# Kernel tuning notes

Measured on AMD Instinct MI355X. Metric: run time of the kernel, lower is better.

Reference implementation:

```python
import jax, jax.numpy as jnp
import numpy as np

E = 768   # embedding_dim
D = 64    # head_dim
B = 8
S = 2048


def setup_inputs() -> dict:
    key = jax.random.key(0)
    k1, k2, k3, k4 = jax.random.split(key, 4)
    inputs = jax.random.normal(k1, (B, S, E), dtype=jnp.float32)
    # causal mask: 1 where attending allowed, 0 elsewhere (masked_fill where ==0)
    attention_mask = jnp.tril(jnp.ones((S, S), dtype=jnp.int32))[None, :, :]
    Q = jax.random.normal(k2, (E, D), dtype=jnp.float32) * 0.01
    K = jax.random.normal(k3, (E, D), dtype=jnp.float32) * 0.01
    V = jax.random.normal(k4, (E, D), dtype=jnp.float32) * 0.01
    return {"inputs": inputs, "attention_mask": attention_mask, "Q": Q, "K": K, "V": V}


def reference(inputs, attention_mask, Q, K, V):
    scale = 1.0 / np.sqrt(D).astype(np.float32)
    q = inputs @ Q          # [B,S,D]
    k = inputs @ K          # [B,S,D]
    v = inputs @ V          # [B,S,D]
    w = jnp.einsum('bqd,bkd->bqk', q, k) * scale   # [B,S,S]
    w = jnp.where(attention_mask == 0, -jnp.inf, w)
    attn = jax.nn.softmax(w, axis=-1)              # [B,S,S]
    states = attn @ v                              # [B,S,D] (dropout p=0.0 is identity)
    return states
```

## Files before the change

kernel.cpp:

```cpp
#include <hip/hip_runtime.h>
#include <cstdint>

#define B_ 8
#define S_ 2048
#define E_ 768
#define D_ 64
#define NSPLIT 4
#define SEGLEN (S_ / NSPLIT)
#define ROWS (B_ * S_)

typedef unsigned short ushort_t;
typedef __attribute__((ext_vector_type(8))) short s16x8;
typedef __attribute__((ext_vector_type(4))) float f32x4;

__device__ inline ushort_t f2bf(float f) {
  unsigned int x = __float_as_uint(f);
  return (ushort_t)((x + 0x7fffu + ((x >> 16) & 1u)) >> 16);
}

__device__ inline unsigned int pkbf(float hi, float lo) {
  return __builtin_amdgcn_perm(__float_as_uint(hi) + 0x8000u,
                               __float_as_uint(lo) + 0x8000u, 0x07060302u);
}

__device__ inline void async16(const void* g, void* l) {
  __builtin_amdgcn_global_load_lds(
      (const __attribute__((address_space(1))) unsigned int*)g,
      (__attribute__((address_space(3))) unsigned int*)l, 16, 0, 0);
}

__global__ __launch_bounds__(256) void wt_kernel(
    const float* __restrict__ Wq, const float* __restrict__ Wk,
    const float* __restrict__ Wv, ushort_t* __restrict__ wt) {
  const int mat = blockIdx.y;
  const int e = blockIdx.x * 4 + (threadIdx.x >> 6);
  const int d = threadIdx.x & 63;
  const float* W = (mat == 0) ? Wq : ((mat == 1) ? Wk : Wv);
  wt[(long)(mat * 64 + d) * E_ + e] = f2bf(W[(long)e * D_ + d]);
}

__global__ __launch_bounds__(256) void qkv_mfma(
    const float* __restrict__ in, const ushort_t* __restrict__ wt,
    ushort_t* __restrict__ qb, ushort_t* __restrict__ kb,
    ushort_t* __restrict__ vtb) {
  const int tid = threadIdx.x;
  const int w = tid >> 6;
  const int L = tid & 63;
  const int c = L & 15;
  const int q = L >> 4;
  const int row0 = blockIdx.x * 32;

  __shared__ float Alds[2][32][64];
  __shared__ ushort_t Blds[2][192][64];

  const int ar0 = w * 8 + (L >> 4);
  const int ar1 = ar0 + 4;
  const int asl = L & 15;
  const float* asrc0 = in + (long)(row0 + ar0) * E_ + ((asl ^ (ar0 & 15)) << 2);
  const float* asrc1 = in + (long)(row0 + ar1) * E_ + ((asl ^ (ar1 & 15)) << 2);
  const int bsl = L & 7;
  const ushort_t* bsrc[6];
#pragma unroll
  for (int jj = 0; jj < 6; ++jj) {
    const int br = w * 48 + jj * 8 + (L >> 3);
    bsrc[jj] = wt + (long)br * E_ + ((bsl ^ (br & 7)) << 3);
  }
  float* ad[2] = {&Alds[0][w * 8][0], &Alds[1][w * 8][0]};
  ushort_t* bd[2] = {&Blds[0][w * 48][0], &Blds[1][w * 48][0]};

  const int mloc = w & 1;
  const int nbase = (w >> 1) * 6;
  const int ra = mloc * 16 + c;
  const int offA00 = ra * 256 + ((2 * q + 0) ^ c) * 16;
  const int offA01 = ra * 256 + ((2 * q + 1) ^ c) * 16;
  const int offA10 = ra * 256 + ((8 + 2 * q + 0) ^ c) * 16;
  const int offA11 = ra * 256 + ((8 + 2 * q + 1) ^ c) * 16;
  int offB0[6], offB1[6];
#pragma unroll
  for (int t = 0; t < 6; ++t) {
    const int n = (nbase + t) * 16 + c;
    offB0[t] = n * 128 + ((q + 0) ^ (c & 7)) * 16;
    offB1[t] = n * 128 + ((q + 4) ^ (c & 7)) * 16;
  }
  const char* Abase = (const char*)&Alds[0][0][0];
  const char* Bbase = (const char*)&Blds[0][0][0];

  f32x4 acc[6];
#pragma unroll
  for (int n = 0; n < 6; ++n) acc[n] = (f32x4){0.f, 0.f, 0.f, 0.f};

  async16(asrc0, ad[0]);
  async16(asrc1, ad[0] + 4 * 64);
#pragma unroll
  for (int jj = 0; jj < 6; ++jj) async16(bsrc[jj], bd[0] + jj * 8 * 64);
  asrc0 += 64; asrc1 += 64;
#pragma unroll
  for (int jj = 0; jj < 6; ++jj) bsrc[jj] += 64;

  for (int it = 0; it < E_ / 64; ++it) {
    const int b = it & 1;
    __syncthreads();
    if (it + 1 < E_ / 64) {
      const int nb = 1 - b;
      async16(asrc0, ad[nb]);
      async16(asrc1, ad[nb] + 4 * 64);
#pragma unroll
      for (int jj = 0; jj < 6; ++jj) async16(bsrc[jj], bd[nb] + jj * 8 * 64);
      asrc0 += 64; asrc1 += 64;
#pragma unroll
      for (int jj = 0; jj < 6; ++jj) bsrc[jj] += 64;
    }
    const char* Ab = Abase + b * 8192;
    const char* Bb = Bbase + b * 24576;
    const float4 a00 = *(const float4*)(Ab + offA00);
    const float4 a01 = *(const float4*)(Ab + offA01);
    const float4 a10 = *(const float4*)(Ab + offA10);
    const float4 a11 = *(const float4*)(Ab + offA11);
    union { s16x8 v; unsigned int u[4]; } af0, af1;
    af0.u[0] = pkbf(a00.y, a00.x);
    af0.u[1] = pkbf(a00.w, a00.z);
    af0.u[2] = pkbf(a01.y, a01.x);
    af0.u[3] = pkbf(a01.w, a01.z);
    af1.u[0] = pkbf(a10.y, a10.x);
    af1.u[1] = pkbf(a10.w, a10.z);
    af1.u[2] = pkbf(a11.y, a11.x);
    af1.u[3] = pkbf(a11.w, a11.z);
#pragma unroll
    for (int t = 0; t < 6; ++t) {
      const s16x8 bf0 = *(const s16x8*)(Bb + offB0[t]);
      const s16x8 bf1 = *(const s16x8*)(Bb + offB1[t]);
      acc[t] = __builtin_amdgcn_mfma_f32_16x16x32_bf16(af0.v, bf0, acc[t], 0, 0, 0);
      acc[t] = __builtin_amdgcn_mfma_f32_16x16x32_bf16(af1.v, bf1, acc[t], 0, 0, 0);
    }
  }

  const float qscale = 0.125f * 1.44269504088896340736f;
  const int row0w = row0 + mloc * 16;
  const int b_ = row0w >> 11;
  const int srow = row0w & (S_ - 1);
#pragma unroll
  for (int n = 0; n < 6; ++n) {
    const int gn = nbase + n;
    const int mat = gn >> 2;
    const int d0 = (gn & 3) * 16 + c;
#pragma unroll
    for (int reg = 0; reg < 4; ++reg) {
      const int m = q * 4 + reg;
      const float x = acc[n][reg];
      if (mat == 0) {
        qb[(long)(row0w + m) * D_ + d0] = f2bf(x * qscale);
      } else if (mat == 1) {
        kb[(long)(row0w + m) * D_ + d0] = f2bf(x);
      } else {
        vtb[(long)b_ * D_ * S_ + (long)d0 * S_ + srow + m] = f2bf(x);
      }
    }
  }
}

__global__ __launch_bounds__(256) void attn_mfma(
    const ushort_t* __restrict__ qb, const ushort_t* __restrict__ kb,
    const ushort_t* __restrict__ vtb, float* __restrict__ op,
    float* __restrict__ lw) {
  const int qb0 = blockIdx.x * 64;
  const int batch = blockIdx.y;
  const int seg = blockIdx.z;
  const int j0 = seg * SEGLEN;
  const int jmax = min(j0 + SEGLEN, qb0 + 64);
  if (j0 >= jmax) return;
  const int nt64 = (jmax - j0) >> 6;
  const int niter = (nt64 + 1) >> 1;

  const int w = threadIdx.x >> 6;
  const int L = threadIdx.x & 63;
  const int col = L & 15;
  const int quad = L >> 4;

  __shared__ ushort_t Kl[2][2][64][64];
  __shared__ ushort_t Vl[2][2][64][64];
  __shared__ ushort_t Pl[4][16][72];

  const ushort_t* kbb = kb + (long)batch * S_ * D_;
  const ushort_t* vbb = vtb + (long)batch * D_ * S_;

  const int lr = L >> 3;
  const int gsw = (L & 7) ^ lr;
  const ushort_t* ksrc[4];
  const ushort_t* vsrc[4];
  ushort_t* kdst[2][4];
  ushort_t* vdst[2][4];
#pragma unroll
  for (int jj = 0; jj < 4; ++jj) {
    const int i = w * 4 + jj;
    ksrc[jj] = kbb + (long)(j0 + i * 8 + lr) * D_ + gsw * 8;
    vsrc[jj] = vbb + (long)((i & 7) * 8 + lr) * S_ + j0 + (i >> 3) * 64 + gsw * 8;
    kdst[0][jj] = &Kl[0][0][0][0] + i * 512;
    kdst[1][jj] = &Kl[1][0][0][0] + i * 512;
    vdst[0][jj] = &Vl[0][0][0][0] + i * 512;
    vdst[1][jj] = &Vl[1][0][0][0] + i * 512;
  }

  const int s0 = ((quad ^ (col & 7)) * 16);

  const ushort_t* qrow = qb + ((long)(batch * S_ + qb0 + w * 16 + col) * D_);
  const s16x8 qf0 = *(const s16x8*)(qrow + quad * 8);
  const s16x8 qf1 = *(const s16x8*)(qrow + 32 + quad * 8);

  f32x4 O[4];
#pragma unroll
  for (int t = 0; t < 4; ++t) O[t] = (f32x4){0.f, 0.f, 0.f, 0.f};
  float l[4] = {0.f, 0.f, 0.f, 0.f};

#pragma unroll
  for (int jj = 0; jj < 4; ++jj) {
    async16(ksrc[jj], kdst[0][jj]);
    async16(vsrc[jj], vdst[0][jj]);
    ksrc[jj] += 128 * D_;
    vsrc[jj] += 128;
  }

  for (int it = 0; it < niter; ++it) {
    const int b = it & 1;
    __syncthreads();
    if (it + 1 < niter) {
      const int nb = 1 - b;
#pragma unroll
      for (int jj = 0; jj < 4; ++jj) {
        async16(ksrc[jj], kdst[nb][jj]);
        async16(vsrc[jj], vdst[nb][jj]);
        ksrc[jj] += 128 * D_;
        vsrc[jj] += 128;
      }
    }
#pragma unroll
    for (int h = 0; h < 2; ++h) {
      const int t64 = it * 2 + h;
      if (t64 < nt64) {
        const int kt = j0 + t64 * 64;
        const char* Kb = (const char*)&Kl[b][h][0][0];
        const char* Vb = (const char*)&Vl[b][h][0][0];
        f32x4 S[4];
#pragma unroll
        for (int t = 0; t < 4; ++t) {
          const s16x8 kf0 = *(const s16x8*)(Kb + (t * 16 + col) * 128 + s0);
          const s16x8 kf1 = *(const s16x8*)(Kb + (t * 16 + col) * 128 + (s0 ^ 64));
          f32x4 z = (f32x4){0.f, 0.f, 0.f, 0.f};
          z = __builtin_amdgcn_mfma_f32_16x16x32_bf16(qf0, kf0, z, 0, 0, 0);
          S[t] = __builtin_amdgcn_mfma_f32_16x16x32_bf16(qf1, kf1, z, 0, 0, 0);
        }
        if (kt + 64 > qb0) {
#pragma unroll
          for (int t = 0; t < 4; ++t) {
            const int colg = kt + t * 16 + col;
#pragma unroll
            for (int reg = 0; reg < 4; ++reg) {
              const int rowg = qb0 + w * 16 + quad * 4 + reg;
              if (colg > rowg) S[t][reg] = -1e30f;
            }
          }
        }
        float P[4][4];
#pragma unroll
        for (int t = 0; t < 4; ++t)
#pragma unroll
          for (int reg = 0; reg < 4; ++reg) {
            P[t][reg] = exp2f(S[t][reg]);
            l[reg] += P[t][reg];
          }
#pragma unroll
        for (int t = 0; t < 4; ++t)
#pragma unroll
          for (int reg = 0; reg < 4; ++reg)
            Pl[w][quad * 4 + reg][t * 16 + col] = f2bf(P[t][reg]);
        const s16x8 p0 = *(const s16x8*)&Pl[w][col][quad * 8];
        const s16x8 p1 = *(const s16x8*)&Pl[w][col][32 + quad * 8];
#pragma unroll
        for (int t = 0; t < 4; ++t) {
          const s16x8 vf0 = *(const s16x8*)(Vb + (t * 16 + col) * 128 + s0);
          const s16x8 vf1 = *(const s16x8*)(Vb + (t * 16 + col) * 128 + (s0 ^ 64));
          O[t] = __builtin_amdgcn_mfma_f32_16x16x32_bf16(p0, vf0, O[t], 0, 0, 0);
          O[t] = __builtin_amdgcn_mfma_f32_16x16x32_bf16(p1, vf1, O[t], 0, 0, 0);
        }
      }
    }
  }
#pragma unroll
  for (int off = 1; off < 16; off <<= 1)
#pragma unroll
    for (int reg = 0; reg < 4; ++reg)
      l[reg] += __shfl_xor(l[reg], off);

  const int growbase = batch * S_ + qb0 + w * 16;
#pragma unroll
  for (int t = 0; t < 4; ++t)
#pragma unroll
    for (int reg = 0; reg < 4; ++reg)
      op[((long)seg * ROWS + growbase + quad * 4 + reg) * D_ + t * 16 + col] =
          O[t][reg];
  if (col == 0) {
#pragma unroll
    for (int reg = 0; reg < 4; ++reg)
      lw[(long)seg * ROWS + growbase + quad * 4 + reg] = l[reg];
  }
}

__global__ __launch_bounds__(256) void attn_combine(
    const float* __restrict__ op, const float* __restrict__ lw,
    float* __restrict__ out) {
  const int t = threadIdx.x;
  const int d = t & 63;
  const int g = blockIdx.x * 4 + (t >> 6);
  const int s_q = g & (S_ - 1);
  float osum = 0.f, lsum = 0.f;
#pragma unroll
  for (int s = 0; s < NSPLIT; ++s) {
    if (s_q >= s * SEGLEN) {
      osum += op[((long)s * ROWS + g) * D_ + d];
      lsum += lw[(long)s * ROWS + g];
    }
  }
  out[(long)g * D_ + d] = osum / lsum;
}

extern "C" void kernel_launch(void* const* d_in, const int* in_sizes, int n_in,
                              void* d_out, int out_size, void* d_ws, size_t ws_size,
                              hipStream_t stream) {
  const float* in = (const float*)d_in[0];
  const float* Wq = (const float*)d_in[2];
  const float* Wk = (const float*)d_in[3];
  const float* Wv = (const float*)d_in[4];
  float* out = (float*)d_out;

  ushort_t* qbuf = (ushort_t*)d_ws;
  ushort_t* kbuf = qbuf + (long)ROWS * D_;
  ushort_t* vtb = kbuf + (long)ROWS * D_;
  float* op = (float*)(vtb + (long)ROWS * D_);
  float* lw = op + (long)NSPLIT * ROWS * D_;
  ushort_t* wt = (ushort_t*)(lw + (long)NSPLIT * ROWS);

  wt_kernel<<<dim3(E_ / 4, 3), 256, 0, stream>>>(Wq, Wk, Wv, wt);
  qkv_mfma<<<ROWS / 32, 256, 0, stream>>>(in, wt, qbuf, kbuf, vtb);
  attn_mfma<<<dim3(S_ / 64, B_, NSPLIT), 256, 0, stream>>>(qbuf, kbuf, vtb, op, lw);
  attn_combine<<<(ROWS * D_) / 256, 256, 0, stream>>>(op, lw, out);
}
```

Baseline: 141.9 us.

## Give each attention wave 32 query rows and store split partials as bf16

The attention kernel drops from 4 waves to 2 per block. Each wave now handles two 16-row query tiles and reuses the K and V fragments it holds in registers across both, which roughly halves LDS fragment reads per tile. The double buffer now holds one 64-key tile per stage instead of two. Split-K partial outputs are written as bf16 instead of fp32, cutting write and read traffic between the attention and combine kernels. The cost is lower parallelism per block, higher register pressure, and some extra rounding error in the unnormalized partial sums.

```diff
diff --git a/kernel.cpp b/kernel.cpp
--- a/kernel.cpp
+++ b/kernel.cpp
@@ -16,6 +16,11 @@
 __device__ inline ushort_t f2bf(float f) {
   unsigned int x = __float_as_uint(f);
   return (ushort_t)((x + 0x7fffu + ((x >> 16) & 1u)) >> 16);
+}
+
+__device__ inline float bf2f(ushort_t u) {
+  unsigned int x = ((unsigned int)u) << 16;
+  return __uint_as_float(x);
 }
 
 __device__ inline unsigned int pkbf(float hi, float lo) {
@@ -158,9 +163,9 @@
   }
 }
 
-__global__ __launch_bounds__(256) void attn_mfma(
+__global__ __launch_bounds__(128) void attn_mfma(
     const ushort_t* __restrict__ qb, const ushort_t* __restrict__ kb,
-    const ushort_t* __restrict__ vtb, float* __restrict__ op,
+    const ushort_t* __restrict__ vtb, ushort_t* __restrict__ op,
     float* __restrict__ lw) {
   const int qb0 = blockIdx.x * 64;
   const int batch = blockIdx.y;
@@ -168,17 +173,16 @@
   const int j0 = seg * SEGLEN;
   const int jmax = min(j0 + SEGLEN, qb0 + 64);
   if (j0 >= jmax) return;
-  const int nt64 = (jmax - j0) >> 6;
-  const int niter = (nt64 + 1) >> 1;
+  const int ntiles = (jmax - j0) >> 6;
 
   const int w = threadIdx.x >> 6;
   const int L = threadIdx.x & 63;
   const int col = L & 15;
   const int quad = L >> 4;
 
-  __shared__ ushort_t Kl[2][2][64][64];
-  __shared__ ushort_t Vl[2][2][64][64];
-  __shared__ ushort_t Pl[4][16][72];
+  __shared__ ushort_t Kl[2][64][64];
+  __shared__ ushort_t Vl[2][64][64];
+  __shared__ ushort_t Pl[2][16][72];
 
   const ushort_t* kbb = kb + (long)batch * S_ * D_;
   const ushort_t* vbb = vtb + (long)batch * D_ * S_;
@@ -193,119 +197,133 @@
   for (int jj = 0; jj < 4; ++jj) {
     const int i = w * 4 + jj;
     ksrc[jj] = kbb + (long)(j0 + i * 8 + lr) * D_ + gsw * 8;
-    vsrc[jj] = vbb + (long)((i & 7) * 8 + lr) * S_ + j0 + (i >> 3) * 64 + gsw * 8;
-    kdst[0][jj] = &Kl[0][0][0][0] + i * 512;
-    kdst[1][jj] = &Kl[1][0][0][0] + i * 512;
-    vdst[0][jj] = &Vl[0][0][0][0] + i * 512;
-    vdst[1][jj] = &Vl[1][0][0][0] + i * 512;
+    vsrc[jj] = vbb + (long)(i * 8 + lr) * S_ + j0 + gsw * 8;
+    kdst[0][jj] = &Kl[0][0][0] + i * 512;
+    kdst[1][jj] = &Kl[1][0][0] + i * 512;
+    vdst[0][jj] = &Vl[0][0][0] + i * 512;
+    vdst[1][jj] = &Vl[1][0][0] + i * 512;
   }
 
   const int s0 = ((quad ^ (col & 7)) * 16);
 
-  const ushort_t* qrow = qb + ((long)(batch * S_ + qb0 + w * 16 + col) * D_);
-  const s16x8 qf0 = *(const s16x8*)(qrow + quad * 8);
-  const s16x8 qf1 = *(const s16x8*)(qrow + 32 + quad * 8);
-
-  f32x4 O[4];
-#pragma unroll
-  for (int t = 0; t < 4; ++t) O[t] = (f32x4){0.f, 0.f, 0.f, 0.f};
-  float l[4] = {0.f, 0.f, 0.f, 0.f};
+  s16x8 qf[2][2];
+#pragma unroll
+  for (int m = 0; m < 2; ++m) {
+    const ushort_t* qrow =
+        qb + ((long)(batch * S_ + qb0 + w * 32 + m * 16 + col) * D_);
+    qf[m][0] = *(const s16x8*)(qrow + quad * 8);
+    qf[m][1] = *(const s16x8*)(qrow + 32 + quad * 8);
+  }
+
+  f32x4 O[2][4];
+#pragma unroll
+  for (int m = 0; m < 2; ++m)
+#pragma unroll
+    for (int t = 0; t < 4; ++t) O[m][t] = (f32x4){0.f, 0.f, 0.f, 0.f};
+  float l[2][4] = {{0.f, 0.f, 0.f, 0.f}, {0.f, 0.f, 0.f, 0.f}};
 
 #pragma unroll
   for (int jj = 0; jj < 4; ++jj) {
     async16(ksrc[jj], kdst[0][jj]);
     async16(vsrc[jj], vdst[0][jj]);
-    ksrc[jj] += 128 * D_;
-    vsrc[jj] += 128;
-  }
-
-  for (int it = 0; it < niter; ++it) {
-    const int b = it & 1;
+    ksrc[jj] += 64 * D_;
+    vsrc[jj] += 64;
+  }
+
+  for (int i = 0; i < ntiles; ++i) {
+    const int b = i & 1;
+    const int kt = j0 + i * 64;
     __syncthreads();
-    if (it + 1 < niter) {
+    if (i + 1 < ntiles) {
       const int nb = 1 - b;
 #pragma unroll
       for (int jj = 0; jj < 4; ++jj) {
         async16(ksrc[jj], kdst[nb][jj]);
         async16(vsrc[jj], vdst[nb][jj]);
-        ksrc[jj] += 128 * D_;
-        vsrc[jj] += 128;
-      }
-    }
-#pragma unroll
-    for (int h = 0; h < 2; ++h) {
-      const int t64 = it * 2 + h;
-      if (t64 < nt64) {
-        const int kt = j0 + t64 * 64;
-        const char* Kb = (const char*)&Kl[b][h][0][0];
-        const char* Vb = (const char*)&Vl[b][h][0][0];
-        f32x4 S[4];
+        ksrc[jj] += 64 * D_;
+        vsrc[jj] += 64;
+      }
+    }
+    const char* Kb = (const char*)&Kl[b][0][0];
+    const char* Vb = (const char*)&Vl[b][0][0];
+
+    s16x8 kf[4][2], vf[4][2];
+#pragma unroll
+    for (int t = 0; t < 4; ++t) {
+      kf[t][0] = *(const s16x8*)(Kb + (t * 16 + col) * 128 + s0);
+      kf[t][1] = *(const s16x8*)(Kb + (t * 16 + col) * 128 + (s0 ^ 64));
+      vf[t][0] = *(const s16x8*)(Vb + (t * 16 + col) * 128 + s0);
+      vf[t][1] = *(const s16x8*)(Vb + (t * 16 + col) * 128 + (s0 ^ 64));
+    }
+#pragma unroll
+    for (int m = 0; m < 2; ++m) {
+      f32x4 S[4];
+#pragma unroll
+      for (int t = 0; t < 4; ++t) {
+        f32x4 z = (f32x4){0.f, 0.f, 0.f, 0.f};
+        z = __builtin_amdgcn_mfma_f32_16x16x32_bf16(qf[m][0], kf[t][0], z, 0, 0, 0);
+        S[t] = __builtin_amdgcn_mfma_f32_16x16x32_bf16(qf[m][1], kf[t][1], z, 0, 0, 0);
+      }
+      if (kt + 64 > qb0) {
 #pragma unroll
         for (int t = 0; t < 4; ++t) {
-          const s16x8 kf0 = *(const s16x8*)(Kb + (t * 16 + col) * 128 + s0);
-          const s16x8 kf1 = *(const s16x8*)(Kb + (t * 16 + col) * 128 + (s0 ^ 64));
-          f32x4 z = (f32x4){0.f, 0.f, 0.f, 0.f};
-          z = __builtin_amdgcn_mfma_f32_16x16x32_bf16(qf0, kf0, z, 0, 0, 0);
-          S[t] = __builtin_amdgcn_mfma_f32_16x16x32_bf16(qf1, kf1, z, 0, 0, 0);
-        }
-        if (kt + 64 > qb0) {
-#pragma unroll
-          for (int t = 0; t < 4; ++t) {
-            const int colg = kt + t * 16 + col;
-#pragma unroll
-            for (int reg = 0; reg < 4; ++reg) {
-              const int rowg = qb0 + w * 16 + quad * 4 + reg;
-              if (colg > rowg) S[t][reg] = -1e30f;
-            }
+          const int colg = kt + t * 16 + col;
+#pragma unroll
+          for (int reg = 0; reg < 4; ++reg) {
+            const int rowg = qb0 + w * 32 + m * 16 + quad * 4 + reg;
+            if (colg > rowg) S[t][reg] = -1e30f;
           }
         }
-        float P[4][4];
-#pragma unroll
-        for (int t = 0; t < 4; ++t)
-#pragma unroll
-          for (int reg = 0; reg < 4; ++reg) {
-            P[t][reg] = exp2f(S[t][reg]);
-            l[reg] += P[t][reg];
-          }
-#pragma unroll
-        for (int t = 0; t < 4; ++t)
-#pragma unroll
-          for (int reg = 0; reg < 4; ++reg)
-            Pl[w][quad * 4 + reg][t * 16 + col] = f2bf(P[t][reg]);
-        const s16x8 p0 = *(const s16x8*)&Pl[w][col][quad * 8];
-        const s16x8 p1 = *(const s16x8*)&Pl[w][col][32 + quad * 8];
-#pragma unroll
-        for (int t = 0; t < 4; ++t) {
-          const s16x8 vf0 = *(const s16x8*)(Vb + (t * 16 + col) * 128 + s0);
-          const s16x8 vf1 = *(const s16x8*)(Vb + (t * 16 + col) * 128 + (s0 ^ 64));
-          O[t] = __builtin_amdgcn_mfma_f32_16x16x32_bf16(p0, vf0, O[t], 0, 0, 0);
-          O[t] = __builtin_amdgcn_mfma_f32_16x16x32_bf16(p1, vf1, O[t], 0, 0, 0);
+      }
+      float P[4][4];
+#pragma unroll
+      for (int t = 0; t < 4; ++t)
+#pragma unroll
+        for (int reg = 0; reg < 4; ++reg) {
+          P[t][reg] = exp2f(S[t][reg]);
+          l[m][reg] += P[t][reg];
         }
+#pragma unroll
+      for (int t = 0; t < 4; ++t)
+#pragma unroll
+        for (int reg = 0; reg < 4; ++reg)
+          Pl[w][quad * 4 + reg][t * 16 + col] = f2bf(P[t][reg]);
+      const s16x8 p0 = *(const s16x8*)&Pl[w][col][quad * 8];
+      const s16x8 p1 = *(const s16x8*)&Pl[w][col][32 + quad * 8];
+#pragma unroll
+      for (int t = 0; t < 4; ++t) {
+        O[m][t] = __builtin_amdgcn_mfma_f32_16x16x32_bf16(p0, vf[t][0], O[m][t], 0, 0, 0);
+        O[m][t] = __builtin_amdgcn_mfma_f32_16x16x32_bf16(p1, vf[t][1], O[m][t], 0, 0, 0);
       }
     }
   }
 #pragma unroll
   for (int off = 1; off < 16; off <<= 1)
 #pragma unroll
-    for (int reg = 0; reg < 4; ++reg)
-      l[reg] += __shfl_xor(l[reg], off);
-
-  const int growbase = batch * S_ + qb0 + w * 16;
-#pragma unroll
-  for (int t = 0; t < 4; ++t)
-#pragma unroll
-    for (int reg = 0; reg < 4; ++reg)
-      op[((long)seg * ROWS + growbase + quad * 4 + reg) * D_ + t * 16 + col] =
-          O[t][reg];
-  if (col == 0) {
-#pragma unroll
-    for (int reg = 0; reg < 4; ++reg)
-      lw[(long)seg * ROWS + growbase + quad * 4 + reg] = l[reg];
+    for (int m = 0; m < 2; ++m)
+#pragma unroll
+      for (int reg = 0; reg < 4; ++reg)
+        l[m][reg] += __shfl_xor(l[m][reg], off);
+
+  const long growbase = (long)batch * S_ + qb0 + w * 32;
+#pragma unroll
+  for (int m = 0; m < 2; ++m) {
+#pragma unroll
+    for (int t = 0; t < 4; ++t)
+#pragma unroll
+      for (int reg = 0; reg < 4; ++reg)
+        op[((long)seg * ROWS + growbase + m * 16 + quad * 4 + reg) * D_ +
+           t * 16 + col] = f2bf(O[m][t][reg]);
+    if (col == 0) {
+#pragma unroll
+      for (int reg = 0; reg < 4; ++reg)
+        lw[(long)seg * ROWS + growbase + m * 16 + quad * 4 + reg] = l[m][reg];
+    }
   }
 }
 
 __global__ __launch_bounds__(256) void attn_combine(
-    const float* __restrict__ op, const float* __restrict__ lw,
+    const ushort_t* __restrict__ op, const float* __restrict__ lw,
     float* __restrict__ out) {
   const int t = threadIdx.x;
   const int d = t & 63;
@@ -315,7 +333,7 @@
 #pragma unroll
   for (int s = 0; s < NSPLIT; ++s) {
     if (s_q >= s * SEGLEN) {
-      osum += op[((long)s * ROWS + g) * D_ + d];
+      osum += bf2f(op[((long)s * ROWS + g) * D_ + d]);
       lsum += lw[(long)s * ROWS + g];
     }
   }
@@ -334,12 +352,12 @@
   ushort_t* qbuf = (ushort_t*)d_ws;
   ushort_t* kbuf = qbuf + (long)ROWS * D_;
   ushort_t* vtb = kbuf + (long)ROWS * D_;
-  float* op = (float*)(vtb + (long)ROWS * D_);
-  float* lw = op + (long)NSPLIT * ROWS * D_;
+  ushort_t* op = vtb + (long)ROWS * D_;
+  float* lw = (float*)(op + (long)NSPLIT * ROWS * D_);
   ushort_t* wt = (ushort_t*)(lw + (long)NSPLIT * ROWS);
 
   wt_kernel<<<dim3(E_ / 4, 3), 256, 0, stream>>>(Wq, Wk, Wv, wt);
   qkv_mfma<<<ROWS / 32, 256, 0, stream>>>(in, wt, qbuf, kbuf, vtb);
-  attn_mfma<<<dim3(S_ / 64, B_, NSPLIT), 256, 0, stream>>>(qbuf, kbuf, vtb, op, lw);
+  attn_mfma<<<dim3(S_ / 64, B_, NSPLIT), 128, 0, stream>>>(qbuf, kbuf, vtb, op, lw);
   attn_combine<<<(ROWS * D_) / 256, 256, 0, stream>>>(op, lw, out);
 }
```

Result: no change. 140.3 us (-1.1%).
